# Performance work log

Hardware: AMD Instinct MI355X
Metric: run time of the kernel (lower is better)

The kernel has to match this reference:

```python
import jax, jax.numpy as jnp
import numpy as np

B, T, D = 4, 2048, 512
H, DK = 8, 64  # n_head, d_kv; inner_dim = H*DK = 512


def setup_inputs() -> dict:
    key = jax.random.key(0)
    ks = jax.random.split(key, 6)
    s = 1.0 / np.sqrt(D)
    return {
        "x": jax.random.normal(ks[0], (B, T, D), dtype=jnp.float32),
        "mask": jnp.zeros((B, 1, 1, T), dtype=jnp.float32),
        "position_bias": jax.random.normal(ks[1], (1, H, T, T), dtype=jnp.float32),
        "Wq": jax.random.normal(ks[2], (D, D), dtype=jnp.float32) * s,
        "Wk": jax.random.normal(ks[3], (D, D), dtype=jnp.float32) * s,
        "Wv": jax.random.normal(ks[4], (D, D), dtype=jnp.float32) * s,
        "Wo": jax.random.normal(ks[5], (D, D), dtype=jnp.float32) * s,
    }


def reference(x, mask, position_bias, Wq, Wk, Wv, Wo):
    # Linear projections (torch nn.Linear: y = x @ W.T), split into heads.
    q = (x @ Wq.T).reshape(B, T, H, DK).transpose(0, 2, 1, 3)  # [B,H,T,DK]
    k = (x @ Wk.T).reshape(B, T, H, DK).transpose(0, 2, 1, 3)  # [B,H,S,DK]
    v = (x @ Wv.T).reshape(B, T, H, DK).transpose(0, 2, 1, 3)  # [B,H,S,DK]
    # T5: no 1/sqrt(d_k) scaling; additive position bias + mask before softmax.
    scores = jnp.einsum("bhtd,bhsd->bhts", q, k) + position_bias + mask
    attn = jax.nn.softmax(scores.astype(jnp.float32), axis=-1).astype(q.dtype)
    # dropout is identity at inference
    y = jnp.einsum("bhts,bhsd->bhtd", attn, v)  # [B,H,T,DK]
    y = y.transpose(0, 2, 1, 3).reshape(B, T, H * DK)
    return y @ Wo.T
```

## Files before the change

kernel.cpp:

```cpp
#include <hip/hip_runtime.h>
#include <stdint.h>

typedef unsigned short u16;
typedef __attribute__((ext_vector_type(8))) _Float16 half8;
typedef __attribute__((ext_vector_type(4))) float f32x4;

#define L2E 1.4426950408889634f

#define NTOK 8192
#define DIM  512
#define TT   2048

__device__ __forceinline__ u16 f2h(float f) {
  _Float16 h = (_Float16)f;
  return __builtin_bit_cast(u16, h);
}

__device__ __forceinline__ void async16(const void* g, void* l) {
  __builtin_amdgcn_global_load_lds(
      (const __attribute__((address_space(1))) unsigned int*)g,
      (__attribute__((address_space(3))) unsigned int*)l, 16, 0, 0);
}

__global__ __launch_bounds__(256) void k_convert(
    const float* __restrict__ x, const float* __restrict__ wq,
    const float* __restrict__ wk, const float* __restrict__ wv,
    const float* __restrict__ wo, u16* __restrict__ xb) {
  size_t i = ((size_t)blockIdx.x * 256 + threadIdx.x) * 8;
  const float* src;
  u16* dst;
  size_t off;
  if (i < 4194304) {
    src = x; dst = xb; off = i;
  } else {
    size_t j = i - 4194304;
    int w = (int)(j >> 18);
    off = j & 262143;
    src = (w == 0) ? wq : (w == 1) ? wk : (w == 2) ? wv : wo;
    dst = xb + 4194304 + (size_t)w * 262144;
  }
  float4 a = *(const float4*)(src + off);
  float4 b = *(const float4*)(src + off + 4);
  uint4 pk;
  pk.x = (unsigned)f2h(a.x) | ((unsigned)f2h(a.y) << 16);
  pk.y = (unsigned)f2h(a.z) | ((unsigned)f2h(a.w) << 16);
  pk.z = (unsigned)f2h(b.x) | ((unsigned)f2h(b.y) << 16);
  pk.w = (unsigned)f2h(b.z) | ((unsigned)f2h(b.w) << 16);
  *(uint4*)(dst + off) = pk;
}

template <bool VSWAP>
__global__ __launch_bounds__(256) void k_proj(
    const u16* __restrict__ A, const u16* __restrict__ Wb,
    u16* __restrict__ Db) {
  const int tid = threadIdx.x;
  const int wave = tid >> 6, lane = tid & 63;
  const int quad = lane >> 4, l16 = lane & 15;
  const int wr = wave >> 1, wc = wave & 1;
  const int m0 = blockIdx.x * 128, n0 = blockIdx.y * 128;

  const u16* W;
  u16* D;
  if (VSWAP) {
    W = Wb + 2 * 262144;
    D = Db + 2 * (size_t)4194304;
  } else {
    int z = blockIdx.z;
    W = Wb + (size_t)z * 262144;
    D = Db + (size_t)z * 4194304;
  }

  __shared__ __align__(16) u16 As[128 * 64];
  __shared__ __align__(16) u16 Bs[128 * 64];

  f32x4 acc[4][4];
  for (int rt = 0; rt < 4; ++rt)
    for (int ct = 0; ct < 4; ++ct) acc[rt][ct] = (f32x4){0.f, 0.f, 0.f, 0.f};

  for (int kb = 0; kb < 8; ++kb) {
    const int k0 = kb * 64;
    for (int r = 0; r < 4; ++r) {
      int cid = r * 256 + tid;
      int row = cid >> 3, cl = cid & 7, cg = cl ^ (row & 7);
      async16(A + (size_t)(m0 + row) * DIM + k0 + cg * 8,
              &As[(r * 256 + wave * 64) * 8]);
    }
    for (int r = 0; r < 4; ++r) {
      int cid = r * 256 + tid;
      int row = cid >> 3, cl = cid & 7, cg = cl ^ (row & 7);
      async16(W + (size_t)(n0 + row) * DIM + k0 + cg * 8,
              &Bs[(r * 256 + wave * 64) * 8]);
    }
    __syncthreads();
    for (int kc = 0; kc < 2; ++kc) {
      half8 af[4], wf[4];
      for (int rt = 0; rt < 4; ++rt) {
        int row = wr * 64 + rt * 16 + l16;
        int c = (kc * 4 + quad) ^ (row & 7);
        af[rt] = *(const half8*)&As[row * 64 + c * 8];
      }
      for (int ct = 0; ct < 4; ++ct) {
        int row = wc * 64 + ct * 16 + l16;
        int c = (kc * 4 + quad) ^ (row & 7);
        wf[ct] = *(const half8*)&Bs[row * 64 + c * 8];
      }
      for (int rt = 0; rt < 4; ++rt)
        for (int ct = 0; ct < 4; ++ct)
          acc[rt][ct] = VSWAP
              ? __builtin_amdgcn_mfma_f32_16x16x32_f16(wf[ct], af[rt],
                                                       acc[rt][ct], 0, 0, 0)
              : __builtin_amdgcn_mfma_f32_16x16x32_f16(af[rt], wf[ct],
                                                       acc[rt][ct], 0, 0, 0);
    }
    __syncthreads();
  }

  for (int rt = 0; rt < 4; ++rt)
    for (int ct = 0; ct < 4; ++ct)
      for (int reg = 0; reg < 4; ++reg) {
        float v = acc[rt][ct][reg];
        if (!VSWAP) {
          int gm = m0 + wr * 64 + rt * 16 + quad * 4 + reg;
          int gn = n0 + wc * 64 + ct * 16 + l16;
          int bb = gm >> 11, t = gm & 2047, hh = gn >> 6, dk = gn & 63;
          D[(((size_t)(bb * 8 + hh) * TT + t) << 6) + dk] = f2h(v);
        } else {
          int feat = n0 + wc * 64 + ct * 16 + quad * 4 + reg;
          int tok  = m0 + wr * 64 + rt * 16 + l16;
          int bb = tok >> 11, t = tok & 2047, hh = feat >> 6, dk = feat & 63;
          D[(((size_t)(bb * 8 + hh) << 6) + dk) * TT + t] = f2h(v);
        }
      }
}

__global__ __launch_bounds__(256) void k_ogemm(
    const u16* __restrict__ A, const u16* __restrict__ W,
    float* __restrict__ Df) {
  const int tid = threadIdx.x;
  const int wave = tid >> 6, lane = tid & 63;
  const int quad = lane >> 4, l16 = lane & 15;
  const int wr = wave >> 1, wc = wave & 1;
  const int m0 = blockIdx.x * 64, n0 = blockIdx.y * 128;

  __shared__ __align__(16) u16 As[64 * 64];
  __shared__ __align__(16) u16 Bs[128 * 64];

  f32x4 acc[2][4];
  for (int rt = 0; rt < 2; ++rt)
    for (int ct = 0; ct < 4; ++ct) acc[rt][ct] = (f32x4){0.f, 0.f, 0.f, 0.f};

  for (int kb = 0; kb < 8; ++kb) {
    const int k0 = kb * 64;
    for (int r = 0; r < 2; ++r) {
      int cid = r * 256 + tid;
      int row = cid >> 3, cl = cid & 7, cg = cl ^ (row & 7);
      async16(A + (size_t)(m0 + row) * DIM + k0 + cg * 8,
              &As[(r * 256 + wave * 64) * 8]);
    }
    for (int r = 0; r < 4; ++r) {
      int cid = r * 256 + tid;
      int row = cid >> 3, cl = cid & 7, cg = cl ^ (row & 7);
      async16(W + (size_t)(n0 + row) * DIM + k0 + cg * 8,
              &Bs[(r * 256 + wave * 64) * 8]);
    }
    __syncthreads();
    for (int kc = 0; kc < 2; ++kc) {
      half8 af[2], wf[4];
      for (int rt = 0; rt < 2; ++rt) {
        int row = wr * 32 + rt * 16 + l16;
        int c = (kc * 4 + quad) ^ (row & 7);
        af[rt] = *(const half8*)&As[row * 64 + c * 8];
      }
      for (int ct = 0; ct < 4; ++ct) {
        int row = wc * 64 + ct * 16 + l16;
        int c = (kc * 4 + quad) ^ (row & 7);
        wf[ct] = *(const half8*)&Bs[row * 64 + c * 8];
      }
      for (int rt = 0; rt < 2; ++rt)
        for (int ct = 0; ct < 4; ++ct)
          acc[rt][ct] = __builtin_amdgcn_mfma_f32_16x16x32_f16(
              af[rt], wf[ct], acc[rt][ct], 0, 0, 0);
    }
    __syncthreads();
  }

  for (int rt = 0; rt < 2; ++rt)
    for (int ct = 0; ct < 4; ++ct)
      for (int reg = 0; reg < 4; ++reg) {
        int gm = m0 + wr * 32 + rt * 16 + quad * 4 + reg;
        int gn = n0 + wc * 64 + ct * 16 + l16;
        Df[(size_t)gm * DIM + gn] = acc[rt][ct][reg];
      }
}

__global__ __launch_bounds__(256) void k_attn(
    const u16* __restrict__ Q, const u16* __restrict__ K,
    const u16* __restrict__ Vt, const float* __restrict__ bias,
    const float* __restrict__ mask, u16* __restrict__ Y) {
  const int tid = threadIdx.x;
  const int wv = tid >> 6;
  const int lane = tid & 63;
  const int quad = lane >> 4;
  const int l16 = lane & 15;

  const int bx = blockIdx.x;
  const int bh = bx >> 5;
  const int qt = bx & 31;
  const int b = bh >> 3, h = bh & 7;
  const int q0 = qt * 64;

  __shared__ __align__(16) u16 Ks[64 * 64];
  __shared__ __align__(16) u16 Vs[64 * 64];
  __shared__ __align__(16) u16 Pl[64 * 72];

  half8 qf[2];
  {
    size_t qrow = (size_t)bh * TT + q0 + wv * 16 + l16;
    for (int kc = 0; kc < 2; ++kc)
      qf[kc] = *(const half8*)(Q + qrow * 64 + kc * 32 + quad * 8);
  }

  float m_i[4], l_i[4];
  f32x4 oacc[4];
  for (int r = 0; r < 4; ++r) { m_i[r] = -1e30f; l_i[r] = 0.f; }
  for (int ct = 0; ct < 4; ++ct) oacc[ct] = (f32x4){0.f, 0.f, 0.f, 0.f};

  const size_t biasbase = (size_t)h * TT * TT;

  for (int st = 0; st < 32; ++st) {
    const int s0 = st * 64;
    for (int r = 0; r < 2; ++r) {
      int cid = r * 256 + tid;
      int row = cid >> 3, cl = cid & 7, cg = cl ^ (row & 7);
      async16(K + ((size_t)bh * TT + s0 + row) * 64 + cg * 8,
              &Ks[(r * 256 + wv * 64) * 8]);
      async16(Vt + ((size_t)(bh * 64 + row)) * TT + s0 + cg * 8,
              &Vs[(r * 256 + wv * 64) * 8]);
    }
    __syncthreads();

    float mk[4];
    for (int ct = 0; ct < 4; ++ct) mk[ct] = mask[b * TT + s0 + ct * 16 + l16];

    f32x4 sacc[4];
    for (int ct = 0; ct < 4; ++ct) sacc[ct] = (f32x4){0.f, 0.f, 0.f, 0.f};
    for (int kc = 0; kc < 2; ++kc) {
      half8 kf[4];
      for (int ct = 0; ct < 4; ++ct) {
        int row = ct * 16 + l16;
        int c = (kc * 4 + quad) ^ (row & 7);
        kf[ct] = *(const half8*)&Ks[row * 64 + c * 8];
      }
      for (int ct = 0; ct < 4; ++ct)
        sacc[ct] = __builtin_amdgcn_mfma_f32_16x16x32_f16(
            qf[kc], kf[ct], sacc[ct], 0, 0, 0);
    }

    float bv[4][4];
    {
      int tg = q0 + wv * 16 + quad * 4;
      for (int reg = 0; reg < 4; ++reg) {
        const float* bp = bias + biasbase + (size_t)(tg + reg) * TT + s0 + l16;
        for (int ct = 0; ct < 4; ++ct) bv[ct][reg] = bp[ct * 16];
      }
    }

    for (int reg = 0; reg < 4; ++reg) {
      float s[4];
      for (int ct = 0; ct < 4; ++ct)
        s[ct] = sacc[ct][reg] + bv[ct][reg] + mk[ct];
      float mx = fmaxf(fmaxf(s[0], s[1]), fmaxf(s[2], s[3]));
      mx = fmaxf(mx, __shfl_xor(mx, 1));
      mx = fmaxf(mx, __shfl_xor(mx, 2));
      mx = fmaxf(mx, __shfl_xor(mx, 4));
      mx = fmaxf(mx, __shfl_xor(mx, 8));
      float mold = m_i[reg];
      float mnew = fmaxf(mold, mx);
      float alpha = __builtin_amdgcn_exp2f((mold - mnew) * L2E);
      float p[4], rs = 0.f;
      for (int ct = 0; ct < 4; ++ct) {
        p[ct] = __builtin_amdgcn_exp2f((s[ct] - mnew) * L2E);
        rs += p[ct];
      }
      rs += __shfl_xor(rs, 1);
      rs += __shfl_xor(rs, 2);
      rs += __shfl_xor(rs, 4);
      rs += __shfl_xor(rs, 8);
      l_i[reg] = l_i[reg] * alpha + rs;
      m_i[reg] = mnew;
      for (int ct = 0; ct < 4; ++ct) oacc[ct][reg] *= alpha;
      int prow = wv * 16 + quad * 4 + reg;
      for (int ct = 0; ct < 4; ++ct) Pl[prow * 72 + ct * 16 + l16] = f2h(p[ct]);
    }
    __syncthreads();

    for (int kc = 0; kc < 2; ++kc) {
      half8 pf, vf[4];
      pf = *(const half8*)&Pl[(wv * 16 + l16) * 72 + kc * 32 + quad * 8];
      for (int ct = 0; ct < 4; ++ct) {
        int row = ct * 16 + l16;
        int c = (kc * 4 + quad) ^ (row & 7);
        vf[ct] = *(const half8*)&Vs[row * 64 + c * 8];
      }
      for (int ct = 0; ct < 4; ++ct)
        oacc[ct] = __builtin_amdgcn_mfma_f32_16x16x32_f16(
            pf, vf[ct], oacc[ct], 0, 0, 0);
    }
    __syncthreads();
  }

  for (int reg = 0; reg < 4; ++reg) {
    int tg = q0 + wv * 16 + quad * 4 + reg;
    float inv = 1.f / l_i[reg];
    for (int ct = 0; ct < 4; ++ct) {
      float v = oacc[ct][reg] * inv;
      Y[((size_t)(b * TT + tg)) * DIM + h * 64 + ct * 16 + l16] = f2h(v);
    }
  }
}

extern "C" void kernel_launch(void* const* d_in, const int* in_sizes, int n_in,
                              void* d_out, int out_size, void* d_ws, size_t ws_size,
                              hipStream_t stream) {
  const float* x    = (const float*)d_in[0];
  const float* mask = (const float*)d_in[1];
  const float* bias = (const float*)d_in[2];
  const float* Wq   = (const float*)d_in[3];
  const float* Wk   = (const float*)d_in[4];
  const float* Wv   = (const float*)d_in[5];
  const float* Wo   = (const float*)d_in[6];
  (void)Wk; (void)Wv;

  u16* xb  = (u16*)d_ws;
  u16* wb  = xb + 4194304;
  u16* qkv = wb + 4 * 262144;
  u16* yb  = qkv + 3 * (size_t)4194304;

  k_convert<<<2560, 256, 0, stream>>>(x, Wq, Wk, Wv, Wo, xb);
  k_proj<false><<<dim3(64, 4, 2), 256, 0, stream>>>(xb, wb, qkv);
  k_proj<true><<<dim3(64, 4), 256, 0, stream>>>(xb, wb, qkv);
  k_attn<<<1024, 256, 0, stream>>>(qkv, qkv + 4194304,
                                   qkv + 2 * (size_t)4194304, bias, mask, yb);
  k_ogemm<<<dim3(128, 4), 256, 0, stream>>>(yb, wb + 3 * 262144, (float*)d_out);
}
```

Baseline: 329.4 us.

## Double-buffer K/V tiles and prefetch bias in attention; merge QKV projection launches

```diff
diff --git a/kernel.cpp b/kernel.cpp
--- a/kernel.cpp
+++ b/kernel.cpp
@@ -49,26 +49,20 @@
   *(uint4*)(dst + off) = pk;
 }
 
-template <bool VSWAP>
 __global__ __launch_bounds__(256) void k_proj(
-    const u16* __restrict__ A, const u16* __restrict__ Wb,
+    const u16* __restrict__ A, const u16* __restrict__ Wall,
     u16* __restrict__ Db) {
   const int tid = threadIdx.x;
   const int wave = tid >> 6, lane = tid & 63;
   const int quad = lane >> 4, l16 = lane & 15;
   const int wr = wave >> 1, wc = wave & 1;
-  const int m0 = blockIdx.x * 128, n0 = blockIdx.y * 128;
-
-  const u16* W;
-  u16* D;
-  if (VSWAP) {
-    W = Wb + 2 * 262144;
-    D = Db + 2 * (size_t)4194304;
-  } else {
-    int z = blockIdx.z;
-    W = Wb + (size_t)z * 262144;
-    D = Db + (size_t)z * 4194304;
-  }
+  const int m0 = blockIdx.x * 128;
+  const int n0g = blockIdx.y * 128;
+  const int z = n0g >> 9;
+  const int n0 = n0g & 511;
+
+  const u16* W = Wall + (size_t)n0g * DIM;
+  u16* D = Db + (size_t)z * 4194304;
 
   __shared__ __align__(16) u16 As[128 * 64];
   __shared__ __align__(16) u16 Bs[128 * 64];
@@ -88,7 +82,7 @@
     for (int r = 0; r < 4; ++r) {
       int cid = r * 256 + tid;
       int row = cid >> 3, cl = cid & 7, cg = cl ^ (row & 7);
-      async16(W + (size_t)(n0 + row) * DIM + k0 + cg * 8,
+      async16(W + (size_t)row * DIM + k0 + cg * 8,
               &Bs[(r * 256 + wave * 64) * 8]);
     }
     __syncthreads();
@@ -104,13 +98,17 @@
         int c = (kc * 4 + quad) ^ (row & 7);
         wf[ct] = *(const half8*)&Bs[row * 64 + c * 8];
       }
-      for (int rt = 0; rt < 4; ++rt)
-        for (int ct = 0; ct < 4; ++ct)
-          acc[rt][ct] = VSWAP
-              ? __builtin_amdgcn_mfma_f32_16x16x32_f16(wf[ct], af[rt],
-                                                       acc[rt][ct], 0, 0, 0)
-              : __builtin_amdgcn_mfma_f32_16x16x32_f16(af[rt], wf[ct],
-                                                       acc[rt][ct], 0, 0, 0);
+      if (z != 2) {
+        for (int rt = 0; rt < 4; ++rt)
+          for (int ct = 0; ct < 4; ++ct)
+            acc[rt][ct] = __builtin_amdgcn_mfma_f32_16x16x32_f16(
+                af[rt], wf[ct], acc[rt][ct], 0, 0, 0);
+      } else {
+        for (int rt = 0; rt < 4; ++rt)
+          for (int ct = 0; ct < 4; ++ct)
+            acc[rt][ct] = __builtin_amdgcn_mfma_f32_16x16x32_f16(
+                wf[ct], af[rt], acc[rt][ct], 0, 0, 0);
+      }
     }
     __syncthreads();
   }
@@ -119,7 +117,7 @@
     for (int ct = 0; ct < 4; ++ct)
       for (int reg = 0; reg < 4; ++reg) {
         float v = acc[rt][ct][reg];
-        if (!VSWAP) {
+        if (z != 2) {
           int gm = m0 + wr * 64 + rt * 16 + quad * 4 + reg;
           int gn = n0 + wc * 64 + ct * 16 + l16;
           int bb = gm >> 11, t = gm & 2047, hh = gn >> 6, dk = gn & 63;
@@ -204,13 +202,15 @@
   const int l16 = lane & 15;
 
   const int bx = blockIdx.x;
-  const int bh = bx >> 5;
-  const int qt = bx & 31;
-  const int b = bh >> 3, h = bh & 7;
+  const int b = bx & 3;
+  const int rest = bx >> 2;
+  const int h = rest >> 5;
+  const int qt = rest & 31;
+  const int bh = b * 8 + h;
   const int q0 = qt * 64;
 
-  __shared__ __align__(16) u16 Ks[64 * 64];
-  __shared__ __align__(16) u16 Vs[64 * 64];
+  __shared__ __align__(16) u16 Ks[2][64 * 64];
+  __shared__ __align__(16) u16 Vs[2][64 * 64];
   __shared__ __align__(16) u16 Pl[64 * 72];
 
   half8 qf[2];
@@ -220,27 +220,52 @@
       qf[kc] = *(const half8*)(Q + qrow * 64 + kc * 32 + quad * 8);
   }
 
+  const int tg = q0 + wv * 16 + quad * 4;
+  const float* bb0 = bias + (size_t)h * TT * TT + (size_t)tg * TT + l16;
+  const float* mbase = mask + (size_t)b * TT + l16;
+
   float m_i[4], l_i[4];
   f32x4 oacc[4];
   for (int r = 0; r < 4; ++r) { m_i[r] = -1e30f; l_i[r] = 0.f; }
   for (int ct = 0; ct < 4; ++ct) oacc[ct] = (f32x4){0.f, 0.f, 0.f, 0.f};
 
-  const size_t biasbase = (size_t)h * TT * TT;
+  float bv[2][4][4];
+  float mk[2][4];
+
+  {
+    for (int r = 0; r < 2; ++r) {
+      int cid = r * 256 + tid;
+      int row = cid >> 3, cl = cid & 7, cg = cl ^ (row & 7);
+      async16(K + ((size_t)bh * TT + row) * 64 + cg * 8,
+              &Ks[0][(r * 256 + wv * 64) * 8]);
+      async16(Vt + ((size_t)(bh * 64 + row)) * TT + cg * 8,
+              &Vs[0][(r * 256 + wv * 64) * 8]);
+    }
+    for (int reg = 0; reg < 4; ++reg)
+      for (int ct = 0; ct < 4; ++ct)
+        bv[0][ct][reg] = bb0[(size_t)reg * TT + ct * 16];
+    for (int ct = 0; ct < 4; ++ct) mk[0][ct] = mbase[ct * 16];
+  }
+  __syncthreads();
 
   for (int st = 0; st < 32; ++st) {
-    const int s0 = st * 64;
-    for (int r = 0; r < 2; ++r) {
-      int cid = r * 256 + tid;
-      int row = cid >> 3, cl = cid & 7, cg = cl ^ (row & 7);
-      async16(K + ((size_t)bh * TT + s0 + row) * 64 + cg * 8,
-              &Ks[(r * 256 + wv * 64) * 8]);
-      async16(Vt + ((size_t)(bh * 64 + row)) * TT + s0 + cg * 8,
-              &Vs[(r * 256 + wv * 64) * 8]);
-    }
-    __syncthreads();
-
-    float mk[4];
-    for (int ct = 0; ct < 4; ++ct) mk[ct] = mask[b * TT + s0 + ct * 16 + l16];
+    const int cur = st & 1;
+    if (st < 31) {
+      const int nxt = cur ^ 1;
+      const int s1 = (st + 1) * 64;
+      for (int r = 0; r < 2; ++r) {
+        int cid = r * 256 + tid;
+        int row = cid >> 3, cl = cid & 7, cg = cl ^ (row & 7);
+        async16(K + ((size_t)bh * TT + s1 + row) * 64 + cg * 8,
+                &Ks[nxt][(r * 256 + wv * 64) * 8]);
+        async16(Vt + ((size_t)(bh * 64 + row)) * TT + s1 + cg * 8,
+                &Vs[nxt][(r * 256 + wv * 64) * 8]);
+      }
+      for (int reg = 0; reg < 4; ++reg)
+        for (int ct = 0; ct < 4; ++ct)
+          bv[nxt][ct][reg] = bb0[(size_t)reg * TT + s1 + ct * 16];
+      for (int ct = 0; ct < 4; ++ct) mk[nxt][ct] = mbase[s1 + ct * 16];
+    }
 
     f32x4 sacc[4];
     for (int ct = 0; ct < 4; ++ct) sacc[ct] = (f32x4){0.f, 0.f, 0.f, 0.f};
@@ -249,26 +274,17 @@
       for (int ct = 0; ct < 4; ++ct) {
         int row = ct * 16 + l16;
         int c = (kc * 4 + quad) ^ (row & 7);
-        kf[ct] = *(const half8*)&Ks[row * 64 + c * 8];
+        kf[ct] = *(const half8*)&Ks[cur][row * 64 + c * 8];
       }
       for (int ct = 0; ct < 4; ++ct)
         sacc[ct] = __builtin_amdgcn_mfma_f32_16x16x32_f16(
             qf[kc], kf[ct], sacc[ct], 0, 0, 0);
     }
 
-    float bv[4][4];
-    {
-      int tg = q0 + wv * 16 + quad * 4;
-      for (int reg = 0; reg < 4; ++reg) {
-        const float* bp = bias + biasbase + (size_t)(tg + reg) * TT + s0 + l16;
-        for (int ct = 0; ct < 4; ++ct) bv[ct][reg] = bp[ct * 16];
-      }
-    }
-
     for (int reg = 0; reg < 4; ++reg) {
       float s[4];
       for (int ct = 0; ct < 4; ++ct)
-        s[ct] = sacc[ct][reg] + bv[ct][reg] + mk[ct];
+        s[ct] = sacc[ct][reg] + bv[cur][ct][reg] + mk[cur][ct];
       float mx = fmaxf(fmaxf(s[0], s[1]), fmaxf(s[2], s[3]));
       mx = fmaxf(mx, __shfl_xor(mx, 1));
       mx = fmaxf(mx, __shfl_xor(mx, 2));
@@ -300,7 +316,7 @@
       for (int ct = 0; ct < 4; ++ct) {
         int row = ct * 16 + l16;
         int c = (kc * 4 + quad) ^ (row & 7);
-        vf[ct] = *(const half8*)&Vs[row * 64 + c * 8];
+        vf[ct] = *(const half8*)&Vs[cur][row * 64 + c * 8];
       }
       for (int ct = 0; ct < 4; ++ct)
         oacc[ct] = __builtin_amdgcn_mfma_f32_16x16x32_f16(
@@ -310,11 +326,11 @@
   }
 
   for (int reg = 0; reg < 4; ++reg) {
-    int tg = q0 + wv * 16 + quad * 4 + reg;
+    int tgr = q0 + wv * 16 + quad * 4 + reg;
     float inv = 1.f / l_i[reg];
     for (int ct = 0; ct < 4; ++ct) {
       float v = oacc[ct][reg] * inv;
-      Y[((size_t)(b * TT + tg)) * DIM + h * 64 + ct * 16 + l16] = f2h(v);
+      Y[((size_t)(b * TT + tgr)) * DIM + h * 64 + ct * 16 + l16] = f2h(v);
     }
   }
 }
@@ -337,8 +353,7 @@
   u16* yb  = qkv + 3 * (size_t)4194304;
 
   k_convert<<<2560, 256, 0, stream>>>(x, Wq, Wk, Wv, Wo, xb);
-  k_proj<false><<<dim3(64, 4, 2), 256, 0, stream>>>(xb, wb, qkv);
-  k_proj<true><<<dim3(64, 4), 256, 0, stream>>>(xb, wb, qkv);
+  k_proj<<<dim3(64, 12), 256, 0, stream>>>(xb, wb, qkv);
   k_attn<<<1024, 256, 0, stream>>>(qkv, qkv + 4194304,
                                    qkv + 2 * (size_t)4194304, bias, mask, yb);
   k_ogemm<<<dim3(128, 4), 256, 0, stream>>>(yb, wb + 3 * 262144, (float*)d_out);
```

Result: slower. 529.8 us (+60.9%).
